# Kernel optimization log

Hardware: AMD Instinct MI355X
Metric: run time of the kernel (lower is better)

The kernel has to match this reference:

```python
import jax, jax.numpy as jnp
import numpy as np
import math

E = 65536        # neighbor pairs (edges)
NAT = 2048       # atoms
NRAD = 24        # radial basis size
ZETA = [1, 2, 3, 4]
NCOMP = len(ZETA) + 1  # radial components: one 2-body + one per zeta
RCUT = 6.0
NELEM = 94       # one-hot element encoding size
EMB = 16         # species embedding dim


def _tables():
    """Static lxlylz enumeration per zeta: triples with lx+ly+lz = n, n in 0..z,
    multinomial/binomial normalization and (-1)^n lambda sign."""
    f = np.vectorize(math.factorial)
    tabs = []
    for z in ZETA:
        L = []
        for n in range(z + 1):
            for lx in range(n + 1):
                for ly in range(n - lx + 1):
                    L.append((lx, ly, n - lx - ly))
        L = np.array(L, np.int64)              # [K,3]
        nsum = L.sum(1)                        # [K]
        fact_lxlylz = f(L[:, 0]) * f(L[:, 1]) * f(L[:, 2])
        # (nfact/fact_lxlylz) * z!/((z-n)! n!) = z! / ((z-n)! * lx!ly!lz!)
        fact_norm = math.factorial(z) / (f(z - nsum) * fact_lxlylz)
        lam = (-1.0) ** nsum
        tabs.append((jnp.asarray(L, jnp.float32),
                     jnp.asarray(fact_norm, jnp.float32),
                     jnp.asarray(lam, jnp.float32)))
    return tabs

TABS = _tables()


def _forward(rij, Wr1, br1, Wr2, br2, Ws1, bs1, Ws2, bs2,
             Wa1, ba1, Wa2, ba2, Wa3, ba3, first_atom_idx, species_idx):
    nat = species_idx.shape[0]
    r = jnp.linalg.norm(rij, axis=1)                       # [E]
    u = rij / r[:, None]                                   # [E,3] unit vectors
    fc = 0.5 * (jnp.cos(jnp.pi * jnp.minimum(r, RCUT) / RCUT) + 1.0)
    centers = jnp.linspace(0.0, RCUT, NRAD, dtype=jnp.float32)
    width = RCUT / NRAD
    basis = jnp.exp(-((r[:, None] - centers) ** 2) / (2.0 * width * width)) * fc[:, None]  # [E,NRAD]
    # learned radial functions -> [E, NRAD, NCOMP]
    h = jax.nn.silu(basis @ Wr1 + br1)
    radial = jax.nn.silu(h @ Wr2 + br2).reshape(-1, NRAD, NCOMP)
    seg = first_atom_idx
    # two-body descriptor
    feats = [jax.ops.segment_sum(radial[:, :, 0], seg, num_segments=nat)]  # [nat,NRAD]
    for iz, z in enumerate(ZETA):
        L, fnorm, lam = TABS[iz]
        # g_ij over lxlylz combos: prod of powers of unit-vector components
        g_ij = jnp.prod((u[:, None, :] + 1e-12) ** L[None, :, :], axis=-1) * fnorm  # [E,K]
        g = jnp.einsum('er,ek->erk', radial[:, :, iz + 1], g_ij)                    # [E,NRAD,K]
        gi = jax.ops.segment_sum(g, seg, num_segments=nat)                          # [nat,NRAD,K]
        g2 = gi * gi
        norm = 2.0 ** (1.0 - z)
        feats.append(jnp.sum(g2, axis=-1) * norm)          # lambda = +1
        feats.append(jnp.sum(g2 * lam, axis=-1) * norm)    # lambda = -1
    feat = jnp.concatenate(feats, axis=1)                  # [nat, NRAD*(1+2*nzeta)]
    # species embedding and correlation
    onehot = jax.nn.one_hot(species_idx, NELEM, dtype=feat.dtype)
    emb = jax.nn.silu(onehot @ Ws1 + bs1) @ Ws2 + bs2      # [nat,EMB]
    x = (feat[:, :, None] * emb[:, None, :]).reshape(nat, -1)  # [nat, F*EMB]
    h = jax.nn.silu(x @ Wa1 + ba1)
    h = jax.nn.silu(h @ Wa2 + ba2)
    e = h @ Wa3 + ba3                                      # [nat,1] atomic energies
    return jnp.sum(e)                                      # total energy


def setup_inputs() -> dict:
    key = jax.random.key(0)
    ks = jax.random.split(key, 12)
    def w(k, shp):
        return jax.random.normal(k, shp, jnp.float32) / np.float32(np.sqrt(shp[0]))
    F = NRAD * (1 + 2 * len(ZETA)) * EMB  # 3456
    return {
        "rij": jax.random.normal(ks[0], (E, 3), jnp.float32) * 2.0,
        "Wr1": w(ks[1], (NRAD, 64)), "br1": jnp.zeros((64,), jnp.float32),
        "Wr2": w(ks[2], (64, NCOMP * NRAD)), "br2": jnp.zeros((NCOMP * NRAD,), jnp.float32),
        "Ws1": w(ks[3], (NELEM, 32)), "bs1": jnp.zeros((32,), jnp.float32),
        "Ws2": w(ks[4], (32, EMB)), "bs2": jnp.zeros((EMB,), jnp.float32),
        "Wa1": w(ks[5], (F, 256)), "ba1": jnp.zeros((256,), jnp.float32),
        "Wa2": w(ks[6], (256, 128)), "ba2": jnp.zeros((128,), jnp.float32),
        "Wa3": w(ks[7], (128, 1)), "ba3": jnp.zeros((1,), jnp.float32),
        "first_atom_idx": jnp.sort(jax.random.randint(ks[8], (E,), 0, NAT)),
        "species_idx": jax.random.randint(ks[9], (NAT,), 0, NELEM),
    }


def reference(rij, Wr1, br1, Wr2, br2, Ws1, bs1, Ws2, bs2,
              Wa1, ba1, Wa2, ba2, Wa3, ba3, first_atom_idx, species_idx):
    return _forward(rij, Wr1, br1, Wr2, br2, Ws1, bs1, Ws2, bs2,
                    Wa1, ba1, Wa2, ba2, Wa3, ba3, first_atom_idx, species_idx)
```

## Files before the change

kernel.cpp:

```cpp
#include <hip/hip_runtime.h>
#include <math.h>

#define KTOT 69
#define NRADC 24
#define NFEAT 216
#define NELEMC 94
#define EMBC 16
#define H1C 256
#define H2C 128
#define CE 8

__device__ __constant__ int c_lx[KTOT] = {
  0,0,0,1,
  0,0,0,1,0,0,0,1,1,2,
  0,0,0,1,0,0,0,1,1,2,0,0,0,0,1,1,1,2,2,3,
  0,0,0,1,0,0,0,1,1,2,0,0,0,0,1,1,1,2,2,3,0,0,0,0,0,1,1,1,1,2,2,2,3,3,4};
__device__ __constant__ int c_ly[KTOT] = {
  0,0,1,0,
  0,0,1,0,0,1,2,0,1,0,
  0,0,1,0,0,1,2,0,1,0,0,1,2,3,0,1,2,0,1,0,
  0,0,1,0,0,1,2,0,1,0,0,1,2,3,0,1,2,0,1,0,0,1,2,3,4,0,1,2,3,0,1,2,0,1,0};
__device__ __constant__ int c_lz[KTOT] = {
  0,1,0,0,
  0,1,0,0,2,1,0,1,0,0,
  0,1,0,0,2,1,0,1,0,0,3,2,1,0,2,1,0,1,0,0,
  0,1,0,0,2,1,0,1,0,0,3,2,1,0,2,1,0,1,0,0,4,3,2,1,0,3,2,1,0,2,1,0,1,0,0};
__device__ __constant__ float c_fn[KTOT] = {
  1,1,1,1,
  1,2,2,2,1,2,1,2,2,1,
  1,3,3,3,3,6,3,6,6,3,1,3,3,1,3,6,3,3,3,1,
  1,4,4,4,6,12,6,12,12,6,4,12,12,4,12,24,12,12,12,4,
  1,4,6,4,1,4,12,12,4,6,12,6,4,4,1};
__device__ __constant__ float c_lam[KTOT] = {
  1,-1,-1,-1,
  1,-1,-1,-1,1,1,1,1,1,1,
  1,-1,-1,-1,1,1,1,1,1,1,-1,-1,-1,-1,-1,-1,-1,-1,-1,-1,
  1,-1,-1,-1,1,1,1,1,1,1,-1,-1,-1,-1,-1,-1,-1,-1,-1,-1,
  1,1,1,1,1,1,1,1,1,1,1,1,1,1,1};
__device__ __constant__ int c_zid[KTOT] = {
  0,0,0,0,
  1,1,1,1,1,1,1,1,1,1,
  2,2,2,2,2,2,2,2,2,2,2,2,2,2,2,2,2,2,2,2,
  3,3,3,3,3,3,3,3,3,3,3,3,3,3,3,3,3,3,3,3,3,3,3,3,3,3,3,3,3,3,3,3,3,3,3};
__device__ __constant__ int c_k0[4] = {0,4,14,34};
__device__ __constant__ int c_kn[4] = {4,10,20,35};
__device__ __constant__ float c_zn[4] = {1.0f, 0.5f, 0.25f, 0.125f};

__device__ __forceinline__ float silu(float x) { return x / (1.0f + expf(-x)); }
__device__ __forceinline__ float4 silu4(float4 v) {
  v.x = silu(v.x); v.y = silu(v.y); v.z = silu(v.z); v.w = silu(v.w); return v;
}
__device__ __forceinline__ void fma4(float4& a, float s, const float4 w) {
  a.x += s * w.x; a.y += s * w.y; a.z += s * w.z; a.w += s * w.w;
}

template <int NQ>
__device__ __forceinline__ void edge_layer2(
    const float* __restrict__ s_h, const float* __restrict__ Wr2,
    const float* __restrict__ br2, float4* __restrict__ radial4,
    int e, int og, int eg, int E) {
  float4 acc[NQ];
  const float4* b2 = (const float4*)(br2 + og * 32);
  #pragma unroll
  for (int q = 0; q < NQ; ++q) acc[q] = b2[q];
  #pragma unroll 2
  for (int j = 0; j < 64; ++j) {
    float hv = s_h[e * 65 + j];
    const float4* w = (const float4*)(Wr2 + j * 120 + og * 32);
    #pragma unroll
    for (int q = 0; q < NQ; ++q) fma4(acc[q], hv, w[q]);
  }
  if (eg < E) {
    #pragma unroll
    for (int q = 0; q < NQ; ++q)
      radial4[(size_t)(og * 8 + q) * E + eg] = silu4(acc[q]);
  }
}

__global__ __launch_bounds__(256) void k_edge(
    const float* __restrict__ rij,
    const float* __restrict__ Wr1, const float* __restrict__ br1,
    const float* __restrict__ Wr2, const float* __restrict__ br2,
    float4* __restrict__ radial4, int E) {
  __shared__ float s_bas[64 * 25];
  __shared__ float s_h[64 * 65];
  const int tid = threadIdx.x;
  const int e = tid & 63;
  const int og = __builtin_amdgcn_readfirstlane(tid >> 6);
  const int eg = blockIdx.x * 64 + e;

  {
    float x = 0.0f, y = 0.0f, z = 0.0f;
    if (eg < E) { x = rij[eg * 3 + 0]; y = rij[eg * 3 + 1]; z = rij[eg * 3 + 2]; }
    float r = sqrtf(x * x + y * y + z * z);
    float rc = fminf(r, 6.0f);
    float fcv = (eg < E)
        ? 0.5f * (cosf(3.14159265358979323846f * rc * (1.0f / 6.0f)) + 1.0f)
        : 0.0f;
    #pragma unroll
    for (int t = 0; t < 6; ++t) {
      int m = og * 6 + t;
      float d = r - (6.0f / 23.0f) * (float)m;
      s_bas[e * 25 + m] = expf(-8.0f * d * d) * fcv;
    }
  }
  __syncthreads();

  {
    const float4* b1 = (const float4*)(br1 + og * 16);
    float4 acc[4] = {b1[0], b1[1], b1[2], b1[3]};
    #pragma unroll 4
    for (int m = 0; m < NRADC; ++m) {
      float b = s_bas[e * 25 + m];
      const float4* w = (const float4*)(Wr1 + m * 64 + og * 16);
      #pragma unroll
      for (int q = 0; q < 4; ++q) fma4(acc[q], b, w[q]);
    }
    #pragma unroll
    for (int q = 0; q < 4; ++q) {
      float4 v = silu4(acc[q]);
      float* dst = &s_h[e * 65 + og * 16 + 4 * q];
      dst[0] = v.x; dst[1] = v.y; dst[2] = v.z; dst[3] = v.w;
    }
  }
  __syncthreads();

  if (og < 3) edge_layer2<8>(s_h, Wr2, br2, radial4, e, og, eg, E);
  else        edge_layer2<6>(s_h, Wr2, br2, radial4, e, og, eg, E);
}

__global__ __launch_bounds__(256) void k_atom(
    const float* __restrict__ rij,
    const float4* __restrict__ radial4,
    const int* __restrict__ fai,
    float* __restrict__ feat, int E) {
  const int a = blockIdx.x;
  const int tid = threadIdx.x;
  __shared__ float s_rad[CE * 120];
  __shared__ float s_pw[CE * 15];
  __shared__ float s_gij[CE * KTOT];
  __shared__ float s_gi[NRADC * KTOT];
  __shared__ float s_feat[NFEAT];

  int lo = 0, hi = E;
  while (lo < hi) { int mid = (lo + hi) >> 1; if (fai[mid] < a) lo = mid + 1; else hi = mid; }
  const int start = lo;
  hi = E;
  while (lo < hi) { int mid = (lo + hi) >> 1; if (fai[mid] < a + 1) lo = mid + 1; else hi = mid; }
  const int end = lo;

  float acc[7]; int roff[7]; int koff[7]; bool val[7];
  #pragma unroll
  for (int p = 0; p < 7; ++p) {
    int idx = tid + 256 * p;
    val[p] = (idx < NRADC * KTOT);
    int use = val[p] ? idx : 0;
    int rad = use / KTOT;
    int k = use - rad * KTOT;
    roff[p] = rad * 5 + 1 + c_zid[k];
    koff[p] = k;
    acc[p] = 0.0f;
  }
  float acc2b = 0.0f;

  for (int c0 = start; c0 < end; c0 += CE) {
    const int ne = min(CE, end - c0);
    for (int idx = tid; idx < 30 * ne; idx += 256) {
      int o4 = idx / ne;
      int e = idx - o4 * ne;
      float4 v = radial4[(size_t)o4 * E + (c0 + e)];
      float* dst = &s_rad[e * 120 + o4 * 4];
      dst[0] = v.x; dst[1] = v.y; dst[2] = v.z; dst[3] = v.w;
    }
    if (tid < ne) {
      int eg = c0 + tid;
      float x = rij[eg * 3 + 0], y = rij[eg * 3 + 1], z = rij[eg * 3 + 2];
      float r = sqrtf(x * x + y * y + z * z);
      float inv = 1.0f / r;
      float p3[3] = {x * inv + 1e-12f, y * inv + 1e-12f, z * inv + 1e-12f};
      #pragma unroll
      for (int d = 0; d < 3; ++d) {
        float pw = 1.0f;
        #pragma unroll
        for (int n = 0; n < 5; ++n) { s_pw[tid * 15 + d * 5 + n] = pw; pw *= p3[d]; }
      }
    }
    __syncthreads();
    for (int idx = tid; idx < ne * KTOT; idx += 256) {
      int e = idx / KTOT;
      int k = idx - e * KTOT;
      s_gij[e * KTOT + k] = s_pw[e * 15 + c_lx[k]] * s_pw[e * 15 + 5 + c_ly[k]] *
                            s_pw[e * 15 + 10 + c_lz[k]] * c_fn[k];
    }
    __syncthreads();
    for (int e = 0; e < ne; ++e) {
      const float* rr = &s_rad[e * 120];
      const float* gg = &s_gij[e * KTOT];
      #pragma unroll
      for (int p = 0; p < 7; ++p) acc[p] += rr[roff[p]] * gg[koff[p]];
      if (tid < NRADC) acc2b += rr[tid * 5];
    }
    __syncthreads();
  }

  #pragma unroll
  for (int p = 0; p < 7; ++p) if (val[p]) s_gi[tid + 256 * p] = acc[p];
  if (tid < NRADC) s_feat[tid] = acc2b;
  __syncthreads();

  if (tid < 192) {
    int zb = tid / NRADC;
    int rad = tid - zb * NRADC;
    int z = zb >> 1;
    bool neg = zb & 1;
    int k0 = c_k0[z], kn = c_kn[z];
    float s = 0.0f;
    for (int k = k0; k < k0 + kn; ++k) {
      float g = s_gi[rad * KTOT + k];
      float g2 = g * g;
      s += neg ? g2 * c_lam[k] : g2;
    }
    s_feat[NRADC + zb * NRADC + rad] = s * c_zn[z];
  }
  __syncthreads();
  if (tid < NFEAT) feat[(size_t)a * NFEAT + tid] = s_feat[tid];
}

__global__ void k_emb(const float* __restrict__ Ws1, const float* __restrict__ bs1,
                      const float* __restrict__ Ws2, const float* __restrict__ bs2,
                      float* __restrict__ emb) {
  int s = blockIdx.x, t = threadIdx.x;
  __shared__ float hh[32];
  if (t < 32) hh[t] = silu(Ws1[s * 32 + t] + bs1[t]);
  __syncthreads();
  if (t < EMBC) {
    float acc = bs2[t];
    #pragma unroll
    for (int c = 0; c < 32; ++c) acc += hh[c] * Ws2[c * EMBC + t];
    emb[s * EMBC + t] = acc;
  }
}

__global__ __launch_bounds__(256) void k_B(const float* __restrict__ Wa1,
                                           const float* __restrict__ emb,
                                           float* __restrict__ B) {
  const int i = blockIdx.x;
  const int o = threadIdx.x;
  __shared__ float s_emb[NELEMC * EMBC];
  for (int idx = o; idx < NELEMC * EMBC; idx += 256) s_emb[idx] = emb[idx];
  float w[EMBC];
  #pragma unroll
  for (int j = 0; j < EMBC; ++j) w[j] = Wa1[(size_t)(i * EMBC + j) * H1C + o];
  __syncthreads();
  for (int s = 0; s < NELEMC; ++s) {
    float acc = 0.0f;
    #pragma unroll
    for (int j = 0; j < EMBC; ++j) acc += s_emb[s * EMBC + j] * w[j];
    B[((size_t)s * NFEAT + i) * H1C + o] = acc;
  }
}

__global__ void k_sort(const int* __restrict__ sp, int* __restrict__ order, int nat) {
  __shared__ int cnt[NELEMC];
  __shared__ int off[NELEMC];
  int t = threadIdx.x;
  for (int i = t; i < NELEMC; i += 256) cnt[i] = 0;
  __syncthreads();
  for (int a = t; a < nat; a += 256) atomicAdd(&cnt[sp[a]], 1);
  __syncthreads();
  if (t == 0) { int run = 0; for (int s = 0; s < NELEMC; ++s) { off[s] = run; run += cnt[s]; } }
  __syncthreads();
  for (int a = t; a < nat; a += 256) { int pos = atomicAdd(&off[sp[a]], 1); order[pos] = a; }
}

__global__ __launch_bounds__(256) void k_mlp(
    const float* __restrict__ feat, const float* __restrict__ B,
    const float* __restrict__ ba1, const float* __restrict__ Wa2,
    const float* __restrict__ ba2, const float* __restrict__ Wa3,
    const float* __restrict__ ba3, const int* __restrict__ order,
    const int* __restrict__ sp, float* __restrict__ e_out, int nat) {
  const int nb = gridDim.x;
  int rank = blockIdx.x;
  if ((nb & 7) == 0) rank = (blockIdx.x & 7) * (nb >> 3) + (blockIdx.x >> 3);
  const int a = order[rank];
  const int s = sp[a];
  const int t = threadIdx.x;
  __shared__ float s_feat[NFEAT];
  __shared__ float s_h1[H1C];
  __shared__ float s_red[H2C];
  if (t < NFEAT) s_feat[t] = feat[(size_t)a * NFEAT + t];
  __syncthreads();
  {
    double a0 = (double)ba1[t], a1 = 0.0;
    const float* Bp = B + (size_t)s * NFEAT * H1C + t;
    #pragma unroll 4
    for (int i = 0; i < NFEAT; i += 2) {
      a0 += (double)s_feat[i] * (double)Bp[(size_t)i * H1C];
      a1 += (double)s_feat[i + 1] * (double)Bp[(size_t)(i + 1) * H1C];
    }
    s_h1[t] = silu((float)(a0 + a1));
  }
  __syncthreads();
  if (t < H2C) {
    double a0 = (double)ba2[t], a1 = 0.0;
    #pragma unroll 4
    for (int j = 0; j < H1C; j += 2) {
      a0 += (double)s_h1[j] * (double)Wa2[j * H2C + t];
      a1 += (double)s_h1[j + 1] * (double)Wa2[(j + 1) * H2C + t];
    }
    float h2 = silu((float)(a0 + a1));
    s_red[t] = h2 * Wa3[t];
  }
  __syncthreads();
  if (t < 64) {
    float v = s_red[t] + s_red[t + 64];
    for (int o = 32; o; o >>= 1) v += __shfl_down(v, o, 64);
    if (t == 0) e_out[a] = v + ba3[0];
  }
}

__global__ void k_reduce(const float* __restrict__ e_in, float* __restrict__ out, int nat) {
  int t = threadIdx.x;
  double acc = 0.0;
  for (int i = t; i < nat; i += 256) acc += (double)e_in[i];
  for (int o = 32; o; o >>= 1) acc += __shfl_down(acc, o, 64);
  __shared__ double s_par[4];
  if ((t & 63) == 0) s_par[t >> 6] = acc;
  __syncthreads();
  if (t == 0) out[0] = (float)(s_par[0] + s_par[1] + s_par[2] + s_par[3]);
}

extern "C" void kernel_launch(void* const* d_in, const int* in_sizes, int n_in,
                              void* d_out, int out_size, void* d_ws, size_t ws_size,
                              hipStream_t stream) {
  const float* rij = (const float*)d_in[0];
  const float* Wr1 = (const float*)d_in[1];
  const float* br1 = (const float*)d_in[2];
  const float* Wr2 = (const float*)d_in[3];
  const float* br2 = (const float*)d_in[4];
  const float* Ws1 = (const float*)d_in[5];
  const float* bs1 = (const float*)d_in[6];
  const float* Ws2 = (const float*)d_in[7];
  const float* bs2 = (const float*)d_in[8];
  const float* Wa1 = (const float*)d_in[9];
  const float* ba1 = (const float*)d_in[10];
  const float* Wa2 = (const float*)d_in[11];
  const float* ba2 = (const float*)d_in[12];
  const float* Wa3 = (const float*)d_in[13];
  const float* ba3 = (const float*)d_in[14];
  const int* fai = (const int*)d_in[15];
  const int* spc = (const int*)d_in[16];

  const int E = in_sizes[0] / 3;
  const int nat = in_sizes[16];

  float* ws = (float*)d_ws;
  size_t off = 0;
  float* radial = ws + off; off += (size_t)E * 120;
  float* feat = ws + off;   off += (size_t)nat * NFEAT;
  float* emb = ws + off;    off += (size_t)NELEMC * EMBC;
  float* Bm = ws + off;     off += (size_t)NELEMC * NFEAT * H1C;
  float* e_ws = ws + off;   off += (size_t)nat;
  int* order = (int*)(ws + off);

  k_edge<<<(E + 63) / 64, 256, 0, stream>>>(rij, Wr1, br1, Wr2, br2, (float4*)radial, E);
  k_atom<<<nat, 256, 0, stream>>>(rij, (const float4*)radial, fai, feat, E);
  k_emb<<<NELEMC, 64, 0, stream>>>(Ws1, bs1, Ws2, bs2, emb);
  k_B<<<NFEAT, 256, 0, stream>>>(Wa1, emb, Bm);
  k_sort<<<1, 256, 0, stream>>>(spc, order, nat);
  k_mlp<<<nat, 256, 0, stream>>>(feat, Bm, ba1, Wa2, ba2, Wa3, ba3, order, spc, e_ws, nat);
  k_reduce<<<1, 256, 0, stream>>>(e_ws, (float*)d_out, nat);
}
```

Measured before the change: 232.2 us.

## Register-tile atom accumulation over transposed radial and angular shared buffers

Restructures the per-atom reduction in k_atom. Each thread now holds a 4x4 register tile of (radial, lxlylz) accumulators and sweeps edges with float4 loads from transposed shared buffers, replacing seven scalar gathers per edge. The edge chunk grows from 8 to 16 edges and is split into two halves whose partial sums are merged at the end. Angular terms are computed directly in registers from precomputed powers, which removes one shared-memory stage and one barrier per chunk. The cost is more registers, padding for the irregular k grouping, and zero-filled work on short chunks since most atoms have about 32 edges.

New measurement: 245.0 us. +5.5%, slower.

```diff
diff --git a/kernel.cpp b/kernel.cpp
--- a/kernel.cpp
+++ b/kernel.cpp
@@ -8,7 +8,11 @@
 #define EMBC 16
 #define H1C 256
 #define H2C 128
-#define CE 8
+#define CE 16
+#define EPR 20
+#define KGN 18
+#define GSTR 84
+#define GISTR 76
 
 __device__ __constant__ int c_lx[KTOT] = {
   0,0,0,1,
@@ -37,14 +41,10 @@
   1,-1,-1,-1,1,1,1,1,1,1,-1,-1,-1,-1,-1,-1,-1,-1,-1,-1,
   1,-1,-1,-1,1,1,1,1,1,1,-1,-1,-1,-1,-1,-1,-1,-1,-1,-1,
   1,1,1,1,1,1,1,1,1,1,1,1,1,1,1};
-__device__ __constant__ int c_zid[KTOT] = {
-  0,0,0,0,
-  1,1,1,1,1,1,1,1,1,1,
-  2,2,2,2,2,2,2,2,2,2,2,2,2,2,2,2,2,2,2,2,
-  3,3,3,3,3,3,3,3,3,3,3,3,3,3,3,3,3,3,3,3,3,3,3,3,3,3,3,3,3,3,3,3,3,3,3};
 __device__ __constant__ int c_k0[4] = {0,4,14,34};
 __device__ __constant__ int c_kn[4] = {4,10,20,35};
 __device__ __constant__ float c_zn[4] = {1.0f, 0.5f, 0.25f, 0.125f};
+__device__ __constant__ int c_zidg[KGN] = {0, 1,1,1, 2,2,2,2,2, 3,3,3,3,3,3,3,3,3};
 
 __device__ __forceinline__ float silu(float x) { return x / (1.0f + expf(-x)); }
 __device__ __forceinline__ float4 silu4(float4 v) {
@@ -52,6 +52,18 @@
 }
 __device__ __forceinline__ void fma4(float4& a, float s, const float4 w) {
   a.x += s * w.x; a.y += s * w.y; a.z += s * w.z; a.w += s * w.w;
+}
+__device__ __forceinline__ void fma44(float4& a, const float4 x, const float4 y) {
+  a.x += x.x * y.x; a.y += x.y * y.y; a.z += x.z * y.z; a.w += x.w * y.w;
+}
+__device__ __forceinline__ float hsum4(const float4 v) { return (v.x + v.y) + (v.z + v.w); }
+__device__ __forceinline__ float powsel(int l, float p, float p2, float p3, float p4) {
+  float v = 1.0f;
+  v = l >= 1 ? p : v;
+  v = l >= 2 ? p2 : v;
+  v = l >= 3 ? p3 : v;
+  v = l >= 4 ? p4 : v;
+  return v;
 }
 
 template <int NQ>
@@ -129,17 +141,16 @@
   else        edge_layer2<6>(s_h, Wr2, br2, radial4, e, og, eg, E);
 }
 
-__global__ __launch_bounds__(256) void k_atom(
+__global__ __launch_bounds__(256, 4) void k_atom(
     const float* __restrict__ rij,
     const float4* __restrict__ radial4,
     const int* __restrict__ fai,
     float* __restrict__ feat, int E) {
   const int a = blockIdx.x;
   const int tid = threadIdx.x;
-  __shared__ float s_rad[CE * 120];
-  __shared__ float s_pw[CE * 15];
-  __shared__ float s_gij[CE * KTOT];
-  __shared__ float s_gi[NRADC * KTOT];
+  __shared__ __align__(16) float s_radT[120 * EPR];
+  __shared__ __align__(16) float s_gijT[KGN * GSTR];
+  __shared__ __align__(16) float s_gi[NRADC * GISTR];
   __shared__ float s_feat[NFEAT];
 
   int lo = 0, hi = E;
@@ -149,63 +160,114 @@
   while (lo < hi) { int mid = (lo + hi) >> 1; if (fai[mid] < a + 1) lo = mid + 1; else hi = mid; }
   const int end = lo;
 
-  float acc[7]; int roff[7]; int koff[7]; bool val[7];
+  const bool is_tile = tid < 216;
+  const int eh = is_tile ? (tid / 108) : 0;
+  const int tile = is_tile ? (tid % 108) : 0;
+  const int rg = tile % 6;
+  const int kg = tile / 6;
+  const int zz = c_zidg[kg];
+  const int comp0 = rg * 20 + 1 + zz;
+  const bool is_2b = (tid >= 216 && tid < 240);
+  const int rad2b = tid - 216;
+
+  if (tid < 60) {
+    int rr = tid / EPR, e = tid % EPR;
+    int fkg = rr < 2 ? 3 : 17;
+    int fj = rr < 2 ? 2 + rr : 3;
+    s_gijT[fkg * GSTR + fj * EPR + e] = 0.0f;
+  }
+
+  float4 acc[4][4];
   #pragma unroll
-  for (int p = 0; p < 7; ++p) {
-    int idx = tid + 256 * p;
-    val[p] = (idx < NRADC * KTOT);
-    int use = val[p] ? idx : 0;
-    int rad = use / KTOT;
-    int k = use - rad * KTOT;
-    roff[p] = rad * 5 + 1 + c_zid[k];
-    koff[p] = k;
-    acc[p] = 0.0f;
-  }
-  float acc2b = 0.0f;
+  for (int i = 0; i < 4; ++i)
+    #pragma unroll
+    for (int j = 0; j < 4; ++j) acc[i][j] = make_float4(0, 0, 0, 0);
+  float4 acc2b = make_float4(0, 0, 0, 0);
 
   for (int c0 = start; c0 < end; c0 += CE) {
     const int ne = min(CE, end - c0);
-    for (int idx = tid; idx < 30 * ne; idx += 256) {
-      int o4 = idx / ne;
-      int e = idx - o4 * ne;
-      float4 v = radial4[(size_t)o4 * E + (c0 + e)];
-      float* dst = &s_rad[e * 120 + o4 * 4];
-      dst[0] = v.x; dst[1] = v.y; dst[2] = v.z; dst[3] = v.w;
-    }
-    if (tid < ne) {
-      int eg = c0 + tid;
-      float x = rij[eg * 3 + 0], y = rij[eg * 3 + 1], z = rij[eg * 3 + 2];
-      float r = sqrtf(x * x + y * y + z * z);
+    for (int idx = tid; idx < 30 * CE; idx += 256) {
+      int o4 = idx >> 4;
+      int e = idx & 15;
+      float4 v = make_float4(0, 0, 0, 0);
+      if (e < ne) v = radial4[(size_t)o4 * E + (c0 + e)];
+      int c = o4 * 4;
+      s_radT[(c + 0) * EPR + e] = v.x;
+      s_radT[(c + 1) * EPR + e] = v.y;
+      s_radT[(c + 2) * EPR + e] = v.z;
+      s_radT[(c + 3) * EPR + e] = v.w;
+    }
+    {
+      int e = tid >> 4, sub = tid & 15;
+      int eg = c0 + e;
+      bool ev = e < ne;
+      float x = 1.0f, y = 0.0f, z3 = 0.0f;
+      if (ev) { x = rij[eg * 3 + 0]; y = rij[eg * 3 + 1]; z3 = rij[eg * 3 + 2]; }
+      float r = sqrtf(x * x + y * y + z3 * z3);
       float inv = 1.0f / r;
-      float p3[3] = {x * inv + 1e-12f, y * inv + 1e-12f, z * inv + 1e-12f};
+      float px = x * inv + 1e-12f, py = y * inv + 1e-12f, pz = z3 * inv + 1e-12f;
+      float p2x = px * px, p3x = p2x * px, p4x = p2x * p2x;
+      float p2y = py * py, p3y = p2y * py, p4y = p2y * p2y;
+      float p2z = pz * pz, p3z = p2z * pz, p4z = p2z * p2z;
+      int kstart = sub < 5 ? sub * 5 : 25 + (sub - 5) * 4;
+      int kcnt = sub < 5 ? 5 : 4;
+      for (int t = 0; t < kcnt; ++t) {
+        int k = kstart + t;
+        float g = powsel(c_lx[k], px, p2x, p3x, p4x) *
+                  powsel(c_ly[k], py, p2y, p3y, p4y) *
+                  powsel(c_lz[k], pz, p2z, p3z, p4z) * c_fn[k];
+        if (!ev) g = 0.0f;
+        int prow = k + (k < 14 ? 0 : 2);
+        s_gijT[(prow >> 2) * GSTR + (prow & 3) * EPR + e] = g;
+      }
+    }
+    __syncthreads();
+    if (is_tile) {
       #pragma unroll
-      for (int d = 0; d < 3; ++d) {
-        float pw = 1.0f;
+      for (int s = 0; s < 2; ++s) {
+        int e0 = eh * 8 + s * 4;
+        float4 gg[4];
         #pragma unroll
-        for (int n = 0; n < 5; ++n) { s_pw[tid * 15 + d * 5 + n] = pw; pw *= p3[d]; }
+        for (int j = 0; j < 4; ++j)
+          gg[j] = *(const float4*)&s_gijT[kg * GSTR + j * EPR + e0];
+        #pragma unroll
+        for (int i = 0; i < 4; ++i) {
+          float4 rr = *(const float4*)&s_radT[(comp0 + 5 * i) * EPR + e0];
+          #pragma unroll
+          for (int j = 0; j < 4; ++j) fma44(acc[i][j], rr, gg[j]);
+        }
       }
     }
+    if (is_2b) {
+      #pragma unroll
+      for (int e0 = 0; e0 < 16; e0 += 4) {
+        float4 v = *(const float4*)&s_radT[(rad2b * 5) * EPR + e0];
+        acc2b.x += v.x; acc2b.y += v.y; acc2b.z += v.z; acc2b.w += v.w;
+      }
+    }
     __syncthreads();
-    for (int idx = tid; idx < ne * KTOT; idx += 256) {
-      int e = idx / KTOT;
-      int k = idx - e * KTOT;
-      s_gij[e * KTOT + k] = s_pw[e * 15 + c_lx[k]] * s_pw[e * 15 + 5 + c_ly[k]] *
-                            s_pw[e * 15 + 10 + c_lz[k]] * c_fn[k];
-    }
-    __syncthreads();
-    for (int e = 0; e < ne; ++e) {
-      const float* rr = &s_rad[e * 120];
-      const float* gg = &s_gij[e * KTOT];
-      #pragma unroll
-      for (int p = 0; p < 7; ++p) acc[p] += rr[roff[p]] * gg[koff[p]];
-      if (tid < NRADC) acc2b += rr[tid * 5];
-    }
-    __syncthreads();
-  }
-
+  }
+
+  float4 hs[4];
   #pragma unroll
-  for (int p = 0; p < 7; ++p) if (val[p]) s_gi[tid + 256 * p] = acc[p];
-  if (tid < NRADC) s_feat[tid] = acc2b;
+  for (int i = 0; i < 4; ++i)
+    hs[i] = make_float4(hsum4(acc[i][0]), hsum4(acc[i][1]),
+                        hsum4(acc[i][2]), hsum4(acc[i][3]));
+  if (is_tile && eh == 0) {
+    #pragma unroll
+    for (int i = 0; i < 4; ++i)
+      *(float4*)&s_gi[(rg * 4 + i) * GISTR + kg * 4] = hs[i];
+  }
+  if (is_2b) s_feat[rad2b] = hsum4(acc2b);
+  __syncthreads();
+  if (is_tile && eh == 1) {
+    #pragma unroll
+    for (int i = 0; i < 4; ++i) {
+      float4 v = *(const float4*)&s_gi[(rg * 4 + i) * GISTR + kg * 4];
+      v.x += hs[i].x; v.y += hs[i].y; v.z += hs[i].z; v.w += hs[i].w;
+      *(float4*)&s_gi[(rg * 4 + i) * GISTR + kg * 4] = v;
+    }
+  }
   __syncthreads();
 
   if (tid < 192) {
@@ -216,7 +278,8 @@
     int k0 = c_k0[z], kn = c_kn[z];
     float s = 0.0f;
     for (int k = k0; k < k0 + kn; ++k) {
-      float g = s_gi[rad * KTOT + k];
+      int prow = k + (k < 14 ? 0 : 2);
+      float g = s_gi[rad * GISTR + prow];
       float g2 = g * g;
       s += neg ? g2 * c_lam[k] : g2;
     }
```
